# Kernel optimization log

Hardware: AMD Instinct MI355X
Metric: run time of the kernel (lower is better)

Reference implementation:

```python
import jax, jax.numpy as jnp
import numpy as np

B, N, E = 2, 10000, 80000
NODE_DIM, EDGE_DIM = 30, 3
H, VE, EE = 64, 16, 16  # encoder_hidden_dim -> width AND depth of hidden chain


def _mlp_params(key, din, h, dout, prefix):
    k = jax.random.split(key, 6)
    s_in, s_h = 1.0 / np.sqrt(din), 1.0 / np.sqrt(h)
    return {
        prefix + '_Win': jax.random.normal(k[0], (din, h), jnp.float32) * s_in,
        prefix + '_bin': jax.random.normal(k[1], (h,), jnp.float32) * s_in,
        prefix + '_Whid': jax.random.normal(k[2], (h, h, h), jnp.float32) * s_h,  # h stacked hidden Linears
        prefix + '_bhid': jax.random.normal(k[3], (h, h), jnp.float32) * s_h,
        prefix + '_Wout': jax.random.normal(k[4], (h, dout), jnp.float32) * s_h,
        prefix + '_bout': jax.random.normal(k[5], (dout,), jnp.float32) * s_h,
    }


def setup_inputs() -> dict:
    key = jax.random.key(0)
    ks = jax.random.split(key, 8)
    inp = {
        'nodes': jax.random.normal(ks[0], (B, N, NODE_DIM), jnp.float32),
        'globals_': jax.random.normal(ks[1], (B,), jnp.float32),
        'edges': jax.random.normal(ks[2], (B, E, EDGE_DIM), jnp.float32),
        'senders': jax.random.randint(ks[3], (B, E), 0, N, jnp.int32),
        'receivers': jax.random.randint(ks[4], (B, E), 0, N, jnp.int32),
    }
    inp.update(_mlp_params(ks[5], NODE_DIM + 1, H, VE, 'node'))  # +1 global col
    inp.update(_mlp_params(ks[6], EDGE_DIM + 4, H, EE, 'edge'))  # +4 relative feats
    return inp


def _chain(x, Win, b_in, Whid, bhid, Wout, bout):
    # Linear(in,h) -> h x Linear(h,h) -> Linear(h,out); NO nonlinearity (matches source)
    h = x @ Win + b_in
    def step(c, wb):
        W, b = wb
        return c @ W + b, None
    h, _ = jax.lax.scan(step, h, (Whid, bhid))
    return h @ Wout + bout


def reference(nodes, globals_, edges, senders, receivers,
              node_Win, node_bin, node_Whid, node_bhid, node_Wout, node_bout,
              edge_Win, edge_bin, edge_Whid, edge_bhid, edge_Wout, edge_bout):
    Bv, Nv = nodes.shape[0], nodes.shape[1]
    g = jnp.broadcast_to(globals_[:, None, None], (Bv, Nv, 1))
    nodes_g = jnp.concatenate([nodes, g], axis=-1)  # [B,N,node_dim+1]
    pos = nodes_g[..., :3]  # first 3 features are 3D positions
    gather = jax.vmap(lambda p, idx: p[idx])
    s = gather(pos, senders)    # [B,E,3]
    r = gather(pos, receivers)  # [B,E,3]
    d = s - r
    norm = jnp.linalg.norm(d, axis=-1, keepdims=True)
    edges_full = jnp.concatenate([edges, d, norm], axis=-1)  # [B,E,edge_dim+4]
    latent_nodes = _chain(nodes_g, node_Win, node_bin, node_Whid, node_bhid, node_Wout, node_bout)
    latent_edges = _chain(edges_full, edge_Win, edge_bin, edge_Whid, edge_bhid, edge_Wout, edge_bout)
    return latent_nodes, latent_edges
```

## Files before the change

### kernel.cpp

```cpp
#include <hip/hip_runtime.h>

#define NN 10000
#define EE_ 80000
#define NODE_ROWS 20000
#define NODE_BLOCKS 79
#define EDGE_BLOCKS 625

typedef float f4 __attribute__((ext_vector_type(4)));

#define GLD4(g, l) __builtin_amdgcn_global_load_lds(                      \
    (const __attribute__((address_space(1))) void*)(g),                   \
    (__attribute__((address_space(3))) void*)(l), 16, 0, 0)
#define GLD1(g, l) __builtin_amdgcn_global_load_lds(                      \
    (const __attribute__((address_space(1))) void*)(g),                   \
    (__attribute__((address_space(3))) void*)(l), 4, 0, 0)

__global__ __launch_bounds__(256, 1) void chain_kernel(
    const float* __restrict__ nWin, const float* __restrict__ nbin,
    const float* __restrict__ nWhid, const float* __restrict__ nbhid,
    const float* __restrict__ nWout, const float* __restrict__ nbout,
    const float* __restrict__ eWin, const float* __restrict__ ebin,
    const float* __restrict__ eWhid, const float* __restrict__ ebhid,
    const float* __restrict__ eWout, const float* __restrict__ ebout,
    float* __restrict__ ws)
{
  const int tid  = threadIdx.x;
  const int lane = tid & 63;
  const int wv   = __builtin_amdgcn_readfirstlane(tid >> 6);
  const int c = blockIdx.x >> 4;
  const int q = blockIdx.x & 15;
  const float* Win  = c ? eWin  : nWin;
  const float* bin  = c ? ebin  : nbin;
  const float* Whid = c ? eWhid : nWhid;
  const float* bhid = c ? ebhid : nbhid;
  const float* Wout = c ? eWout : nWout;
  const float* bout = c ? ebout : nbout;
  const int din = c ? 7 : 31;
  float* weff = ws + (c ? 512 : 0);

  __shared__ float lds_f[13312];

  const int r4 = lane >> 4, c16 = lane & 15;
  const int oE = r4*64 + ((c16 ^ r4) << 2);
  const int oO = r4*64 + ((c16 ^ (4 | r4)) << 2);
  const int swz = lane & 7;
  const int aw0 = lane*256 + (((4*wv + 0) ^ swz) << 4);
  const int aw1 = lane*256 + (((4*wv + 1) ^ swz) << 4);
  const int aw2 = lane*256 + (((4*wv + 2) ^ swz) << 4);
  const int aw3 = lane*256 + (((4*wv + 3) ^ swz) << 4);
  const int ab  = 16384 + wv*256 + lane*4;
  const int apw = 52224 + lane*16 + wv*4;
  const int apr = 52224 + lane*16;

  float vlane = Wout[lane*16 + q];
  float bpart = 0.f;
  const int kbase = 16*wv;
  float s[16];
  #pragma unroll
  for (int j = 0; j < 16; ++j)
    s[j] = __uint_as_float(__builtin_amdgcn_readlane(__float_as_uint(vlane), kbase + j));

#define STAGE(BF, L) do {                                                 \
    const float* gW_ = Whid + (size_t)(L)*4096 + wv*1024;                 \
    float* lW_ = lds_f + (BF)*4352 + wv*1024;                             \
    GLD4(gW_ +   0 + oE, lW_ +   0);                                      \
    GLD4(gW_ + 256 + oO, lW_ + 256);                                      \
    GLD4(gW_ + 512 + oE, lW_ + 512);                                      \
    GLD4(gW_ + 768 + oO, lW_ + 768);                                      \
    GLD1(bhid + (size_t)(L)*64 + lane, lds_f + (BF)*4352 + 4096 + wv*64); \
  } while (0)

#define CSTEP(OFS, VMC, STAGESTMT) do {                                   \
    STAGESTMT;                                                            \
    asm volatile("s_waitcnt vmcnt(" #VMC ") lgkmcnt(0)" ::: "memory");    \
    __builtin_amdgcn_s_barrier();           \
    f4 f0_, f1_, f2_, f3_; float bb_;                                     \
    asm volatile("ds_read_b128 %0, %5 offset:" #OFS "\n\t"                \
                 "ds_read_b128 %1, %6 offset:" #OFS "\n\t"                \
                 "ds_read_b128 %2, %7 offset:" #OFS "\n\t"                \
                 "ds_read_b128 %3, %8 offset:" #OFS "\n\t"                \
                 "ds_read_b32  %4, %9 offset:" #OFS "\n\t"                \
                 "s_waitcnt lgkmcnt(0)"                                   \
                 : "=&v"(f0_), "=&v"(f1_), "=&v"(f2_), "=&v"(f3_), "=&v"(bb_) \
                 : "v"(aw0), "v"(aw1), "v"(aw2), "v"(aw3), "v"(ab)        \
                 : "memory");                                             \
    __builtin_amdgcn_sched_barrier(0);                                    \
    bpart = __builtin_fmaf(bb_, vlane, bpart);                            \
    float a0_ = __builtin_fmaf(f0_.y, s[1],  f0_.x * s[0]);               \
    a0_ = __builtin_fmaf(f0_.z, s[2],  a0_);                              \
    a0_ = __builtin_fmaf(f0_.w, s[3],  a0_);                              \
    float a1_ = __builtin_fmaf(f1_.y, s[5],  f1_.x * s[4]);               \
    a1_ = __builtin_fmaf(f1_.z, s[6],  a1_);                              \
    a1_ = __builtin_fmaf(f1_.w, s[7],  a1_);                              \
    float a2_ = __builtin_fmaf(f2_.y, s[9],  f2_.x * s[8]);               \
    a2_ = __builtin_fmaf(f2_.z, s[10], a2_);                              \
    a2_ = __builtin_fmaf(f2_.w, s[11], a2_);                              \
    float a3_ = __builtin_fmaf(f3_.y, s[13], f3_.x * s[12]);              \
    a3_ = __builtin_fmaf(f3_.z, s[14], a3_);                              \
    a3_ = __builtin_fmaf(f3_.w, s[15], a3_);                              \
    float acc_ = (a0_ + a1_) + (a2_ + a3_);                               \
    asm volatile("ds_write_b32 %0, %1\n\t"                                \
                 "s_waitcnt lgkmcnt(0)"                                   \
                 :: "v"(apw), "v"(acc_) : "memory");                      \
    __builtin_amdgcn_s_barrier();                   \
    f4 p4_;                                                               \
    asm volatile("ds_read_b128 %0, %1\n\t"                                \
                 "s_waitcnt lgkmcnt(0)"                                   \
                 : "=&v"(p4_) : "v"(apr) : "memory");                     \
    __builtin_amdgcn_sched_barrier(0);                                    \
    vlane = (p4_.x + p4_.y) + (p4_.z + p4_.w);                            \
    _Pragma("unroll")                                                     \
    for (int jj = 0; jj < 16; ++jj)                                       \
      s[jj] = __uint_as_float(__builtin_amdgcn_readlane(                  \
                  __float_as_uint(vlane), kbase + jj));                   \
  } while (0)

  STAGE(0, 63);
  STAGE(1, 62);

  int L = 63;
  #pragma unroll 1
  for (int ii = 0; ii < 20; ++ii) {
    CSTEP(0,     10, STAGE(2, L-2));
    CSTEP(17408, 10, STAGE(0, L-3));
    CSTEP(34816, 10, STAGE(1, L-4));
    L -= 3;
  }
  CSTEP(0,     10, STAGE(2, 1));
  CSTEP(17408, 10, STAGE(0, 0));
  CSTEP(34816, 5,  (void)0);
  CSTEP(0,     0,  (void)0);
#undef CSTEP
#undef STAGE

  if (wv != 0) return;

  float red = __builtin_fmaf(bin[lane], vlane, bpart);
  #pragma unroll
  for (int off = 32; off > 0; off >>= 1) red += __shfl_xor(red, off, 64);

  float* sv = lds_f;
  sv[lane] = vlane;
  __builtin_amdgcn_sched_barrier(0);

  if (lane == din) {
    weff[din*16 + q] = red + bout[q];
  } else if (lane < din) {
    float a0 = 0.f, a1 = 0.f, a2 = 0.f, a3 = 0.f;
    const float* wr = Win + (size_t)lane*64;
    #pragma unroll
    for (int kb = 0; kb < 16; ++kb) {
      f4 vv = *(const f4*)&sv[kb*4];
      f4 wv4 = *(const f4*)&wr[kb*4];
      a0 = __builtin_fmaf(wv4.x, vv.x, a0);
      a1 = __builtin_fmaf(wv4.y, vv.y, a1);
      a2 = __builtin_fmaf(wv4.z, vv.z, a2);
      a3 = __builtin_fmaf(wv4.w, vv.w, a3);
    }
    weff[lane*16 + q] = (a0 + a1) + (a2 + a3);
  }
}

template<int NF>
static __device__ __forceinline__ void mlp_apply_store(const float* x, const float* sW,
                                                       float* po)
{
  float a[16];
  #pragma unroll
  for (int q = 0; q < 16; ++q) a[q] = sW[NF*16 + q];
  #pragma unroll
  for (int j = 0; j < NF; ++j) {
    const float xv = x[j];
    #pragma unroll
    for (int q = 0; q < 16; ++q) a[q] += xv * sW[j*16 + q];
  }
  float4* d = (float4*)po;
  d[0] = make_float4(a[0],  a[1],  a[2],  a[3]);
  d[1] = make_float4(a[4],  a[5],  a[6],  a[7]);
  d[2] = make_float4(a[8],  a[9],  a[10], a[11]);
  d[3] = make_float4(a[12], a[13], a[14], a[15]);
}

__global__ __launch_bounds__(256) void apply_kernel(
    const float* __restrict__ nodes, const float* __restrict__ globals_,
    const float* __restrict__ edges, const int* __restrict__ senders,
    const int* __restrict__ receivers, const float* __restrict__ ws,
    float* __restrict__ out)
{
  __shared__ float sW[32*16];
  const bool is_node = (blockIdx.x < NODE_BLOCKS);
  {
    const float* src = is_node ? ws : ws + 512;
    const int n = is_node ? 32*16 : 8*16;
    for (int j = threadIdx.x; j < n; j += 256) sW[j] = src[j];
  }
  __syncthreads();

  if (is_node) {
    const int rn = blockIdx.x*256 + threadIdx.x;
    if (rn >= NODE_ROWS) return;
    float x[31];
    const float* p = nodes + (size_t)rn*30;
    #pragma unroll
    for (int j = 0; j < 15; ++j) {
      float2 u = *(const float2*)(p + j*2);
      x[2*j]     = u.x;
      x[2*j + 1] = u.y;
    }
    const int b = (rn >= NN) ? 1 : 0;
    x[30] = globals_[b];
    mlp_apply_store<31>(x, sW, out + (size_t)rn*16);
  } else {
    const int re = (blockIdx.x - NODE_BLOCKS)*256 + threadIdx.x;
    const int b = (re >= EE_) ? 1 : 0;
    float x[7];
    const float* ep = edges + (size_t)re*3;
    x[0] = ep[0]; x[1] = ep[1]; x[2] = ep[2];
    const int si = senders[re], ri = receivers[re];
    const float* ps = nodes + ((size_t)(b*NN + si))*30;
    const float* pr = nodes + ((size_t)(b*NN + ri))*30;
    const float dx = ps[0] - pr[0];
    const float dy = ps[1] - pr[1];
    const float dz = ps[2] - pr[2];
    x[3] = dx; x[4] = dy; x[5] = dz;
    x[6] = sqrtf(dx*dx + dy*dy + dz*dz);
    mlp_apply_store<7>(x, sW, out + (size_t)(NODE_ROWS + re)*16);
  }
}

extern "C" void kernel_launch(void* const* d_in, const int* in_sizes, int n_in,
                              void* d_out, int out_size, void* d_ws, size_t ws_size,
                              hipStream_t stream)
{
  const float* nodes    = (const float*)d_in[0];
  const float* globals_ = (const float*)d_in[1];
  const float* edges    = (const float*)d_in[2];
  const int* senders   = (const int*)d_in[3];
  const int* receivers = (const int*)d_in[4];
  const float* nWin  = (const float*)d_in[5];
  const float* nbin  = (const float*)d_in[6];
  const float* nWhid = (const float*)d_in[7];
  const float* nbhid = (const float*)d_in[8];
  const float* nWout = (const float*)d_in[9];
  const float* nbout = (const float*)d_in[10];
  const float* eWin  = (const float*)d_in[11];
  const float* ebin  = (const float*)d_in[12];
  const float* eWhid = (const float*)d_in[13];
  const float* ebhid = (const float*)d_in[14];
  const float* eWout = (const float*)d_in[15];
  const float* ebout = (const float*)d_in[16];
  float* ws  = (float*)d_ws;
  float* out = (float*)d_out;

  chain_kernel<<<32, 256, 0, stream>>>(
      nWin, nbin, nWhid, nbhid, nWout, nbout,
      eWin, ebin, eWhid, ebhid, eWout, ebout, ws);

  apply_kernel<<<NODE_BLOCKS + EDGE_BLOCKS, 256, 0, stream>>>(
      nodes, globals_, edges, senders, receivers, ws, out);
}
```

Baseline: 45.41 us.

## Pre-multiply hidden layers in parallel chunks of four before the serial fold

Adds a chunk kernel in which 32 blocks each multiply four consecutive 64x64 hidden weight matrices, with their biases, into one affine map. The serial fold kernel then walks 16 combined matrices per chain instead of 64. This cuts the dependent serial chain of the weight collapse to a quarter, at the cost of one extra kernel launch and a workspace round trip. The fold loop counts were adjusted to match (4 iterations plus a tail, starting from layer 15).

```diff
diff --git a/kernel.cpp b/kernel.cpp
--- a/kernel.cpp
+++ b/kernel.cpp
@@ -15,14 +15,96 @@
     (const __attribute__((address_space(1))) void*)(g),                   \
     (__attribute__((address_space(3))) void*)(l), 4, 0, 0)
 
-__global__ __launch_bounds__(256, 1) void chain_kernel(
+__global__ __launch_bounds__(256) void chunk_kernel(
+    const float* __restrict__ nWhid, const float* __restrict__ nbhid,
+    const float* __restrict__ eWhid, const float* __restrict__ ebhid,
+    float* __restrict__ pt)
+{
+  const int t = threadIdx.x;
+  const int c = blockIdx.x >> 4;
+  const int j = blockIdx.x & 15;
+  const float* Wh = c ? eWhid : nWhid;
+  const float* bh = c ? ebhid : nbhid;
+  const int L0 = 4*j;
+
+  __shared__ float s_at[2][64*68];
+  __shared__ float s_b[65*64];
+  __shared__ float s_bp[256];
+
+  for (int idx = t; idx < 4160; idx += 256) {
+    int r = idx >> 6, k = idx & 63;
+    s_at[0][k*68 + r] = (r < 64) ? Wh[(size_t)L0*4096 + idx] : bh[L0*64 + k];
+  }
+  int cur = 0;
+  #pragma unroll 1
+  for (int s = 1; s <= 3; ++s) {
+    const float* WB = Wh + (size_t)(L0 + s)*4096;
+    const float* bB = bh + (size_t)(L0 + s)*64;
+    #pragma unroll
+    for (int i = 0; i < 4; ++i) {
+      int i4 = t + i*256;
+      *(float4*)&s_b[i4*4] = *(const float4*)&WB[i4*4];
+    }
+    if (t < 16) *(float4*)&s_b[4096 + t*4] = *(const float4*)&bB[t*4];
+    __syncthreads();
+
+    const int ti = t >> 4, tj = t & 15;
+    float acc[4][4];
+    #pragma unroll
+    for (int d = 0; d < 4; ++d)
+      #pragma unroll
+      for (int e = 0; e < 4; ++e) acc[d][e] = 0.f;
+    #pragma unroll 4
+    for (int k = 0; k < 64; ++k) {
+      float4 a4 = *(const float4*)&s_at[cur][k*68 + 4*ti];
+      float4 b4 = *(const float4*)&s_b[k*64 + 4*tj];
+      float av[4] = {a4.x, a4.y, a4.z, a4.w};
+      float bv[4] = {b4.x, b4.y, b4.z, b4.w};
+      #pragma unroll
+      for (int d = 0; d < 4; ++d)
+        #pragma unroll
+        for (int e = 0; e < 4; ++e) acc[d][e] += av[d]*bv[e];
+    }
+    {
+      int cc = t & 63, kq = t >> 6;
+      float p = 0.f;
+      #pragma unroll 4
+      for (int kk = 0; kk < 16; ++kk) {
+        int k = kq*16 + kk;
+        p += s_at[cur][k*68 + 64] * s_b[k*64 + cc];
+      }
+      s_bp[kq*64 + cc] = p;
+    }
+    __syncthreads();
+    if (s < 3) {
+      #pragma unroll
+      for (int d = 0; d < 4; ++d)
+        #pragma unroll
+        for (int e = 0; e < 4; ++e)
+          s_at[cur^1][(4*tj + e)*68 + 4*ti + d] = acc[d][e];
+      if (t < 64)
+        s_at[cur^1][t*68 + 64] =
+            s_bp[t] + s_bp[64+t] + s_bp[128+t] + s_bp[192+t] + s_b[4096+t];
+      __syncthreads();
+      cur ^= 1;
+    } else {
+      float* D = pt + (size_t)(c*16 + j)*4160;
+      #pragma unroll
+      for (int d = 0; d < 4; ++d)
+        *(float4*)&D[(4*ti + d)*64 + 4*tj] =
+            make_float4(acc[d][0], acc[d][1], acc[d][2], acc[d][3]);
+      if (t < 64)
+        D[4096 + t] = s_bp[t] + s_bp[64+t] + s_bp[128+t] + s_bp[192+t] + s_b[4096+t];
+    }
+  }
+}
+
+__global__ __launch_bounds__(256, 1) void fold16_kernel(
     const float* __restrict__ nWin, const float* __restrict__ nbin,
-    const float* __restrict__ nWhid, const float* __restrict__ nbhid,
     const float* __restrict__ nWout, const float* __restrict__ nbout,
     const float* __restrict__ eWin, const float* __restrict__ ebin,
-    const float* __restrict__ eWhid, const float* __restrict__ ebhid,
     const float* __restrict__ eWout, const float* __restrict__ ebout,
-    float* __restrict__ ws)
+    const float* __restrict__ pt, float* __restrict__ ws)
 {
   const int tid  = threadIdx.x;
   const int lane = tid & 63;
@@ -31,10 +113,9 @@
   const int q = blockIdx.x & 15;
   const float* Win  = c ? eWin  : nWin;
   const float* bin  = c ? ebin  : nbin;
-  const float* Whid = c ? eWhid : nWhid;
-  const float* bhid = c ? ebhid : nbhid;
   const float* Wout = c ? eWout : nWout;
   const float* bout = c ? ebout : nbout;
+  const float* PT = pt + (size_t)c*16*4160;
   const int din = c ? 7 : 31;
   float* weff = ws + (c ? 512 : 0);
 
@@ -61,13 +142,14 @@
     s[j] = __uint_as_float(__builtin_amdgcn_readlane(__float_as_uint(vlane), kbase + j));
 
 #define STAGE(BF, L) do {                                                 \
-    const float* gW_ = Whid + (size_t)(L)*4096 + wv*1024;                 \
+    const float* gW_ = PT + (size_t)(L)*4160 + wv*1024;                   \
     float* lW_ = lds_f + (BF)*4352 + wv*1024;                             \
     GLD4(gW_ +   0 + oE, lW_ +   0);                                      \
     GLD4(gW_ + 256 + oO, lW_ + 256);                                      \
     GLD4(gW_ + 512 + oE, lW_ + 512);                                      \
     GLD4(gW_ + 768 + oO, lW_ + 768);                                      \
-    GLD1(bhid + (size_t)(L)*64 + lane, lds_f + (BF)*4352 + 4096 + wv*64); \
+    GLD1(PT + (size_t)(L)*4160 + 4096 + lane,                             \
+         lds_f + (BF)*4352 + 4096 + wv*64);                               \
   } while (0)
 
 #define CSTEP(OFS, VMC, STAGESTMT) do {                                   \
@@ -115,12 +197,12 @@
                   __float_as_uint(vlane), kbase + jj));                   \
   } while (0)
 
-  STAGE(0, 63);
-  STAGE(1, 62);
-
-  int L = 63;
+  STAGE(0, 15);
+  STAGE(1, 14);
+
+  int L = 15;
   #pragma unroll 1
-  for (int ii = 0; ii < 20; ++ii) {
+  for (int ii = 0; ii < 4; ++ii) {
     CSTEP(0,     10, STAGE(2, L-2));
     CSTEP(17408, 10, STAGE(0, L-3));
     CSTEP(34816, 10, STAGE(1, L-4));
@@ -251,10 +333,12 @@
   const float* ebout = (const float*)d_in[16];
   float* ws  = (float*)d_ws;
   float* out = (float*)d_out;
-
-  chain_kernel<<<32, 256, 0, stream>>>(
-      nWin, nbin, nWhid, nbhid, nWout, nbout,
-      eWin, ebin, eWhid, ebhid, eWout, ebout, ws);
+  float* pt  = ws + 1024;
+
+  chunk_kernel<<<32, 256, 0, stream>>>(nWhid, nbhid, eWhid, ebhid, pt);
+
+  fold16_kernel<<<32, 256, 0, stream>>>(
+      nWin, nbin, nWout, nbout, eWin, ebin, eWout, ebout, pt, ws);
 
   apply_kernel<<<NODE_BLOCKS + EDGE_BLOCKS, 256, 0, stream>>>(
       nodes, globals_, edges, senders, receivers, ws, out);
```

Measured after the change: 36.91 us, median of 2. 18.7% less time.
